# Kernel tuning notes

Measured on AMD Instinct MI355X. Metric: run time of the kernel, lower is better.

## Reference

```python
import jax, jax.numpy as jnp
import numpy as np

B, C, H, W = 16, 192, 64, 64
L = 256           # number of quantization levels (len(sos.unique_values))
EXTREMA = 10.0    # codebook support roughly [-extrema, extrema]


def setup_inputs() -> dict:
    key = jax.random.key(0)
    k1, k2, k3 = jax.random.split(key, 3)
    inputs = jax.random.normal(k1, (B, C, H, W), dtype=jnp.float32) * 3.0
    means = jax.random.normal(k2, (B, C, H, W), dtype=jnp.float32)
    # sorted codebook of unique quantizer output values (sos.unique_values)
    raw = jax.random.uniform(k3, (L,), dtype=jnp.float32,
                             minval=-EXTREMA, maxval=EXTREMA)
    unique_values = jnp.sort(raw)
    return {"inputs": inputs, "means": means, "unique_values": unique_values}


def _nearest_symbols(v, unique_values):
    # Parallel binary search over the sorted codebook; equivalent to the
    # original per-element argmin(|keys - x|) in transform_map.
    L_ = unique_values.shape[0]
    idx = jnp.searchsorted(unique_values, v)          # in [0, L]
    idx = jnp.clip(idx, 1, L_ - 1)
    left = unique_values[idx - 1]
    right = unique_values[idx]
    # on ties, argmin picks the lower index -> use <=
    return jnp.where(jnp.abs(v - left) <= jnp.abs(v - right), idx - 1, idx)


def reference(inputs, means, unique_values):
    # quantize(mode='symbols'): subtract means, snap to nearest codebook
    # value, map value -> integer symbol via the sorted codebook.
    v = inputs - means
    symbols = _nearest_symbols(v, unique_values)      # int32 [B,C,H,W]
    # dequantize: symbol -> float codebook value (map_cdf_sos), add means.
    dequant = unique_values[symbols] + means          # float32 [B,C,H,W]
    return dequant, symbols
```

## Files before the change

### kernel.cpp

```cpp
#include <hip/hip_runtime.h>


#define LVL 256
#define NB  1024
#define QPT 4

typedef float f32x4 __attribute__((ext_vector_type(4)));

__device__ __forceinline__ int bucket_of(float v, float lo, float scale) {
    int b = (int)floorf((v - lo) * scale);
    return min(max(b, 0), NB - 1);
}

__device__ __forceinline__ int sym_exact(float x, const float* s_uv) {
    int l = 0, h = LVL;
    #pragma unroll
    for (int s = 0; s < 8; ++s) {
        int m = (l + h) >> 1;
        bool r = (s_uv[m] < x);
        l = r ? (m + 1) : l;
        h = r ? h : m;
    }
    int idx = min(max(l, 1), LVL - 1);
    float left = s_uv[idx - 1], right = s_uv[idx];
    return (fabsf(x - left) <= fabsf(x - right)) ? idx - 1 : idx;
}

__device__ __forceinline__ int lb_count(float x, const float* s_uv) {
    int l = 0, h = LVL;
    #pragma unroll
    for (int s = 0; s < 8; ++s) {
        int m = (l + h) >> 1;
        bool r = (s_uv[m] < x);
        l = r ? (m + 1) : l;
        h = r ? h : m;
    }
    return l;
}

__global__ __launch_bounds__(256) void agc_build_lut(
    const float* __restrict__ uv, float4* __restrict__ lut)
{
    __shared__ float s_uv[LVL];
    int t = threadIdx.x;
    s_uv[t] = uv[t];
    __syncthreads();

    const float lo    = s_uv[0];
    const float rng   = s_uv[LVL - 1] - lo;
    const float width = rng / (float)NB;

    #pragma unroll
    for (int q = 0; q < NB / 256; ++q) {
        int b = q * 256 + t;
        float g_lo = lo + (float)(b - 1) * width;
        float g_hi = lo + (float)(b + 2) * width;

        int s1 = (b == 0)      ? 0         : sym_exact(g_lo, s_uv);
        int s2 = (b == NB - 1) ? (LVL - 1) : sym_exact(g_hi, s_uv);

        float4 e;
        if (s2 - s1 <= 1) {
            e.x = s_uv[s1];
            e.y = s_uv[s2];
            e.z = __int_as_float(s1);
            e.w = 0.f;
        } else {
            int A = (b == 0) ? 0 : lb_count(g_lo, s_uv);
            e.x = 0.f; e.y = 0.f;
            e.z = __int_as_float(-(A + 1));
            e.w = 0.f;
        }
        lut[b] = e;
    }
}

__global__ __launch_bounds__(256) void agc_quant_lut(
    const float* __restrict__ inputs,
    const float* __restrict__ means,
    const float* __restrict__ uv,
    const f32x4* __restrict__ lut,
    float* __restrict__ out_deq,
    float* __restrict__ out_sym,
    int n4, int n, int nfull)
{
    const float lo    = uv[0];
    const float scale = (float)NB / (uv[LVL - 1] - lo);

    int t = threadIdx.x;
    const int i0 = blockIdx.x * (256 * QPT) + t;
    const bool full = (blockIdx.x < nfull);

    float4 in[QPT], mn[QPT];
    if (full) {
        #pragma unroll
        for (int k = 0; k < QPT; ++k) {
            int i = i0 + k * 256;
            in[k] = reinterpret_cast<const float4*>(inputs)[i];
            mn[k] = reinterpret_cast<const float4*>(means)[i];
        }
    } else {
        #pragma unroll
        for (int k = 0; k < QPT; ++k) {
            int i = i0 + k * 256;
            if (i < n4) {
                in[k] = reinterpret_cast<const float4*>(inputs)[i];
                mn[k] = reinterpret_cast<const float4*>(means)[i];
            }
        }
    }

    #pragma unroll
    for (int k = 0; k < QPT; ++k) {
        int i = i0 + k * 256;
        if (!full && i >= n4) continue;

        float vs[4] = {in[k].x - mn[k].x, in[k].y - mn[k].y,
                       in[k].z - mn[k].z, in[k].w - mn[k].w};
        float ms[4] = {mn[k].x, mn[k].y, mn[k].z, mn[k].w};
        float dq[4], sy[4];

        int bx[4];
        #pragma unroll
        for (int e = 0; e < 4; ++e) bx[e] = bucket_of(vs[e], lo, scale);

        f32x4 E[4];
        #pragma unroll
        for (int e = 0; e < 4; ++e) E[e] = lut[bx[e]];

        #pragma unroll
        for (int e = 0; e < 4; ++e) {
            float v = vs[e];
            int pk = __float_as_int(E[e].z);

            float val; int sym;
            if (pk >= 0) {
                bool tl = (fabsf(v - E[e].x) <= fabsf(v - E[e].y));
                sym = pk + (tl ? 0 : 1);
                val = tl ? E[e].x : E[e].y;
            } else {
                int s = -pk - 1;
                while (s < LVL && uv[s] < v) ++s;
                int idx = min(max(s, 1), LVL - 1);
                float left  = uv[idx - 1];
                float right = uv[idx];
                bool tl = (fabsf(v - left) <= fabsf(v - right));
                sym = tl ? (idx - 1) : idx;
                val = tl ? left : right;
            }

            sy[e] = (float)sym;
            dq[e] = val + ms[e];
        }

        reinterpret_cast<float4*>(out_deq)[i] = make_float4(dq[0], dq[1], dq[2], dq[3]);
        reinterpret_cast<float4*>(out_sym)[i] = make_float4(sy[0], sy[1], sy[2], sy[3]);
    }

    if (blockIdx.x == 0 && t == 0) {
        for (int j = n4 * 4; j < n; ++j) {
            float m = means[j];
            float v = inputs[j] - m;
            int l = 0, h = LVL;
            for (int s = 0; s < 8; ++s) {
                int mm = (l + h) >> 1;
                bool r = (uv[mm] < v);
                l = r ? (mm + 1) : l;
                h = r ? h : mm;
            }
            int idx = min(max(l, 1), LVL - 1);
            float left = uv[idx - 1], right = uv[idx];
            bool tl = fabsf(v - left) <= fabsf(v - right);
            out_deq[j] = (tl ? left : right) + m;
            out_sym[j] = (float)(tl ? idx - 1 : idx);
        }
    }
}

__global__ __launch_bounds__(256) void agc_quant_fallback(
    const float* __restrict__ inputs,
    const float* __restrict__ means,
    const float* __restrict__ uv,
    float* __restrict__ out_deq,
    float* __restrict__ out_sym,
    int n4, int n)
{
    __shared__ float s_uv[LVL];
    s_uv[threadIdx.x] = uv[threadIdx.x];
    __syncthreads();

    int i = blockIdx.x * blockDim.x + threadIdx.x;
    if (i < n4) {
        float4 in = reinterpret_cast<const float4*>(inputs)[i];
        float4 mn = reinterpret_cast<const float4*>(means)[i];
        float vs[4] = {in.x - mn.x, in.y - mn.y, in.z - mn.z, in.w - mn.w};
        float ms[4] = {mn.x, mn.y, mn.z, mn.w};
        float dq[4], sy[4];
        #pragma unroll
        for (int k = 0; k < 4; ++k) {
            float v = vs[k];
            int lo = 0, hi = LVL;
            #pragma unroll
            for (int s = 0; s < 8; ++s) {
                int mid = (lo + hi) >> 1;
                bool r = (s_uv[mid] < v);
                lo = r ? (mid + 1) : lo;
                hi = r ? hi : mid;
            }
            int idx = min(max(lo, 1), LVL - 1);
            float left = s_uv[idx - 1], right = s_uv[idx];
            bool tl = (fabsf(v - left) <= fabsf(v - right));
            sy[k] = (float)(tl ? idx - 1 : idx);
            dq[k] = (tl ? left : right) + ms[k];
        }
        reinterpret_cast<float4*>(out_deq)[i] = make_float4(dq[0], dq[1], dq[2], dq[3]);
        reinterpret_cast<float4*>(out_sym)[i] = make_float4(sy[0], sy[1], sy[2], sy[3]);
    }
    if (blockIdx.x == 0 && threadIdx.x == 0) {
        for (int j = n4 * 4; j < n; ++j) {
            float m = means[j];
            float v = inputs[j] - m;
            int lo = 0, hi = LVL;
            for (int s = 0; s < 8; ++s) {
                int mid = (lo + hi) >> 1;
                bool r = (s_uv[mid] < v);
                lo = r ? (mid + 1) : lo;
                hi = r ? hi : mid;
            }
            int idx = min(max(lo, 1), LVL - 1);
            float left = s_uv[idx - 1], right = s_uv[idx];
            bool tl = fabsf(v - left) <= fabsf(v - right);
            out_deq[j] = (tl ? left : right) + m;
            out_sym[j] = (float)(tl ? idx - 1 : idx);
        }
    }
}

extern "C" void kernel_launch(void* const* d_in, const int* in_sizes, int n_in,
                              void* d_out, int out_size, void* d_ws, size_t ws_size,
                              hipStream_t stream)
{
    const float* inputs = (const float*)d_in[0];
    const float* means  = (const float*)d_in[1];
    const float* uv     = (const float*)d_in[2];

    int n  = in_sizes[0];
    int n4 = n / 4;

    float* out     = (float*)d_out;
    float* out_deq = out;
    float* out_sym = out + n;

    size_t need = (size_t)NB * sizeof(float4);
    if (d_ws != nullptr && ws_size >= need) {
        float4* lut = (float4*)d_ws;
        agc_build_lut<<<1, 256, 0, stream>>>(uv, lut);

        int per_blk = 256 * QPT;
        int nfull   = n4 / per_blk;
        int blocks  = (n4 + per_blk - 1) / per_blk;
        if (blocks < 1) blocks = 1;
        agc_quant_lut<<<blocks, 256, 0, stream>>>(
            inputs, means, uv, (const f32x4*)lut,
            out_deq, out_sym, n4, n, nfull);
    } else {
        int blocks = (n4 + 255) / 256;
        if (blocks < 1) blocks = 1;
        agc_quant_fallback<<<blocks, 256, 0, stream>>>(
            inputs, means, uv, out_deq, out_sym, n4, n);
    }
}
```

Before: 202.9 us.

## Build LUT from exact midpoint thresholds and use nontemporal input loads

The LUT build now computes, for each adjacent pair of codebook values, the exact float decision threshold by bisecting over the ordered bit pattern. Each histogram bucket then stores how many thresholds fall before and inside it. The build runs across four blocks instead of one. In the quant kernel, buckets that hold several thresholds are resolved by counting thresholds from a small table, replacing the serial scan over the codebook, and the input and means reads use nontemporal loads. This shortens the slow path and the LUT build, at the cost of a little more workspace and a per-thread loop of up to 255 iterations in the build kernel.

```diff
diff --git a/kernel.cpp b/kernel.cpp
--- a/kernel.cpp
+++ b/kernel.cpp
@@ -12,67 +12,65 @@
     return min(max(b, 0), NB - 1);
 }
 
-__device__ __forceinline__ int sym_exact(float x, const float* s_uv) {
-    int l = 0, h = LVL;
-    #pragma unroll
-    for (int s = 0; s < 8; ++s) {
-        int m = (l + h) >> 1;
-        bool r = (s_uv[m] < x);
-        l = r ? (m + 1) : l;
-        h = r ? h : m;
-    }
-    int idx = min(max(l, 1), LVL - 1);
-    float left = s_uv[idx - 1], right = s_uv[idx];
-    return (fabsf(x - left) <= fabsf(x - right)) ? idx - 1 : idx;
-}
-
-__device__ __forceinline__ int lb_count(float x, const float* s_uv) {
-    int l = 0, h = LVL;
-    #pragma unroll
-    for (int s = 0; s < 8; ++s) {
-        int m = (l + h) >> 1;
-        bool r = (s_uv[m] < x);
-        l = r ? (m + 1) : l;
-        h = r ? h : m;
-    }
-    return l;
+__device__ __forceinline__ unsigned f2k(float f) {
+    unsigned u = __float_as_uint(f);
+    return (u & 0x80000000u) ? ~u : (u | 0x80000000u);
+}
+__device__ __forceinline__ float k2f(unsigned k) {
+    unsigned u = (k & 0x80000000u) ? (k & 0x7fffffffu) : ~k;
+    return __uint_as_float(u);
 }
 
 __global__ __launch_bounds__(256) void agc_build_lut(
-    const float* __restrict__ uv, float4* __restrict__ lut)
+    const float* __restrict__ uv, float4* __restrict__ lut, float* __restrict__ thr)
 {
     __shared__ float s_uv[LVL];
+    __shared__ float s_t[LVL];
+    __shared__ int   s_beta[LVL];
     int t = threadIdx.x;
     s_uv[t] = uv[t];
     __syncthreads();
-
     const float lo    = s_uv[0];
-    const float rng   = s_uv[LVL - 1] - lo;
-    const float width = rng / (float)NB;
-
-    #pragma unroll
-    for (int q = 0; q < NB / 256; ++q) {
-        int b = q * 256 + t;
-        float g_lo = lo + (float)(b - 1) * width;
-        float g_hi = lo + (float)(b + 2) * width;
-
-        int s1 = (b == 0)      ? 0         : sym_exact(g_lo, s_uv);
-        int s2 = (b == NB - 1) ? (LVL - 1) : sym_exact(g_hi, s_uv);
-
-        float4 e;
-        if (s2 - s1 <= 1) {
-            e.x = s_uv[s1];
-            e.y = s_uv[s2];
-            e.z = __int_as_float(s1);
-            e.w = 0.f;
+    const float scale = (float)NB / (s_uv[LVL - 1] - lo);
+
+    if (t < LVL - 1) {
+        float a = s_uv[t], b = s_uv[t + 1];
+        float tj;
+        if (a == b) {
+            tj = __builtin_inff();
         } else {
-            int A = (b == 0) ? 0 : lb_count(g_lo, s_uv);
-            e.x = 0.f; e.y = 0.f;
-            e.z = __int_as_float(-(A + 1));
-            e.w = 0.f;
-        }
-        lut[b] = e;
-    }
+            unsigned klo = f2k(a), khi = f2k(b);
+            while (khi - klo > 1u) {
+                unsigned km = klo + (khi - klo) / 2u;
+                float vm = k2f(km);
+                if (fabsf(vm - a) <= fabsf(vm - b)) klo = km; else khi = km;
+            }
+            tj = k2f(khi);
+        }
+        s_t[t]    = tj;
+        s_beta[t] = (tj == __builtin_inff()) ? (NB - 1) : bucket_of(tj, lo, scale);
+        if (blockIdx.x == 0) thr[t] = tj;
+    }
+    __syncthreads();
+
+    int b = blockIdx.x * 256 + t;
+    int A = 0, cnt = 0;
+    for (int j = 0; j < LVL - 1; ++j) {
+        int bj = s_beta[j];
+        A   += (bj <  b);
+        cnt += (bj == b);
+    }
+    float4 e;
+    if (cnt <= 1) {
+        e.x = s_uv[A];
+        e.y = s_uv[A + cnt];
+    } else {
+        e.x = 0.f;
+        e.y = 0.f;
+    }
+    e.z = __int_as_float(A);
+    e.w = __int_as_float(cnt);
+    lut[b] = e;
 }
 
 __global__ __launch_bounds__(256) void agc_quant_lut(
@@ -80,6 +78,7 @@
     const float* __restrict__ means,
     const float* __restrict__ uv,
     const f32x4* __restrict__ lut,
+    const float* __restrict__ thr,
     float* __restrict__ out_deq,
     float* __restrict__ out_sym,
     int n4, int n, int nfull)
@@ -91,21 +90,21 @@
     const int i0 = blockIdx.x * (256 * QPT) + t;
     const bool full = (blockIdx.x < nfull);
 
-    float4 in[QPT], mn[QPT];
+    f32x4 in[QPT], mn[QPT];
     if (full) {
         #pragma unroll
         for (int k = 0; k < QPT; ++k) {
             int i = i0 + k * 256;
-            in[k] = reinterpret_cast<const float4*>(inputs)[i];
-            mn[k] = reinterpret_cast<const float4*>(means)[i];
+            in[k] = __builtin_nontemporal_load(reinterpret_cast<const f32x4*>(inputs) + i);
+            mn[k] = __builtin_nontemporal_load(reinterpret_cast<const f32x4*>(means) + i);
         }
     } else {
         #pragma unroll
         for (int k = 0; k < QPT; ++k) {
             int i = i0 + k * 256;
             if (i < n4) {
-                in[k] = reinterpret_cast<const float4*>(inputs)[i];
-                mn[k] = reinterpret_cast<const float4*>(means)[i];
+                in[k] = __builtin_nontemporal_load(reinterpret_cast<const f32x4*>(inputs) + i);
+                mn[k] = __builtin_nontemporal_load(reinterpret_cast<const f32x4*>(means) + i);
             }
         }
     }
@@ -130,23 +129,21 @@
 
         #pragma unroll
         for (int e = 0; e < 4; ++e) {
-            float v = vs[e];
-            int pk = __float_as_int(E[e].z);
+            float v   = vs[e];
+            int   A   = __float_as_int(E[e].z);
+            int   cnt = __float_as_int(E[e].w);
 
             float val; int sym;
-            if (pk >= 0) {
+            if (cnt <= 1) {
                 bool tl = (fabsf(v - E[e].x) <= fabsf(v - E[e].y));
-                sym = pk + (tl ? 0 : 1);
+                sym = tl ? A : A + 1;
                 val = tl ? E[e].x : E[e].y;
             } else {
-                int s = -pk - 1;
-                while (s < LVL && uv[s] < v) ++s;
-                int idx = min(max(s, 1), LVL - 1);
-                float left  = uv[idx - 1];
-                float right = uv[idx];
-                bool tl = (fabsf(v - left) <= fabsf(v - right));
-                sym = tl ? (idx - 1) : idx;
-                val = tl ? left : right;
+                int s = A;
+                for (int jj = 0; jj < cnt; ++jj)
+                    s += (v >= thr[A + jj]) ? 1 : 0;
+                sym = s;
+                val = uv[s];
             }
 
             sy[e] = (float)sym;
@@ -251,17 +248,18 @@
     float* out_deq = out;
     float* out_sym = out + n;
 
-    size_t need = (size_t)NB * sizeof(float4);
+    size_t need = (size_t)NB * sizeof(float4) + LVL * sizeof(float);
     if (d_ws != nullptr && ws_size >= need) {
         float4* lut = (float4*)d_ws;
-        agc_build_lut<<<1, 256, 0, stream>>>(uv, lut);
+        float*  thr = (float*)((char*)d_ws + (size_t)NB * sizeof(float4));
+        agc_build_lut<<<NB / 256, 256, 0, stream>>>(uv, lut, thr);
 
         int per_blk = 256 * QPT;
         int nfull   = n4 / per_blk;
         int blocks  = (n4 + per_blk - 1) / per_blk;
         if (blocks < 1) blocks = 1;
         agc_quant_lut<<<blocks, 256, 0, stream>>>(
-            inputs, means, uv, (const f32x4*)lut,
+            inputs, means, uv, (const f32x4*)lut, thr,
             out_deq, out_sym, n4, n, nfull);
     } else {
         int blocks = (n4 + 255) / 256;
```

Result: faster. 193.8 us (-4.5%).
